# Kernel optimization log

Measured on AMD Instinct MI355X. Metric: run time of the kernel, lower is better.

The kernel has to match this reference:

```python
import jax, jax.numpy as jnp
import numpy as np

BL = 5
N = 2 ** BL  # 32; LUT is (N+1) x (N+1)


def setup_inputs() -> dict:
    key = jax.random.key(0)
    k1, k2, k3 = jax.random.split(key, 3)
    M, K, O = 512, 256, 256
    x = jax.random.uniform(k1, (M, K), dtype=jnp.float32)              # activations in [0,1)
    W = jax.random.uniform(k2, (O, K), dtype=jnp.float32) * 2.0 - 1.0  # weights in [-1,1)
    b = jax.random.uniform(k3, (O,), dtype=jnp.float32) * 2.0 - 1.0
    # Stochastic-computing multiplication LUT: A[i, j] ~ i*j/N (floored), i,j in [0, N]
    i = np.arange(N + 1, dtype=np.float32)
    lut = jnp.asarray(np.floor(np.outer(i, i) / N), dtype=jnp.float32)
    return {"x": x, "W": W, "b": b, "lut": lut}


def _sanitize(t):
    t = jnp.where(jnp.isnan(t), jnp.zeros_like(t), t)
    return jnp.where(jnp.isinf(t), jnp.ones_like(t), t)


def sc_mat_mac_p(a, b, c, lut, n):
    # Faithful port of SC_MAT_MAC_p: quantize -> LUT gather over all (row, out) pairs ->
    # sign-correct -> reduce over K -> requantize -> add quantized bias -> rescale.
    a = _sanitize(a)
    b = _sanitize(b)
    c = _sanitize(c)
    amax = jnp.abs(a).max()
    amax = jnp.where(amax == 0, jnp.ones_like(amax), amax)
    dmax = jnp.maximum(jnp.abs(b).max(), jnp.abs(c).max())
    dmax = jnp.where(dmax == 0, jnp.ones_like(dmax), dmax)
    # SBL2 = int(log2(int(N / amax))); SN2 = 2**SBL2 (truncations match torch int())
    sn2 = 2.0 ** jnp.floor(jnp.log2(jnp.floor(n / amax)))
    sn1 = 2.0 ** jnp.floor(jnp.log2(jnp.floor(n / dmax)))
    aa = (a * sn2).astype(jnp.int32)  # [M, K], |aa| <= N
    bb = (b * sn1).astype(jnp.int32)  # [O, K], |bb| <= N
    cc = (c * sn1).astype(jnp.int32)  # [O]
    # LUT gather over the full cross product (original materializes this via
    # repeat_interleave/repeat; here it is a broadcasted gather of shape [M, O, K]).
    prod = lut[jnp.abs(aa)[:, None, :], jnp.abs(bb)[None, :, :]]          # [M, O, K]
    sgn = (jnp.sign(aa)[:, None, :] * jnp.sign(bb)[None, :, :]).astype(prod.dtype)
    x9 = (sgn * prod).sum(axis=-1)                                        # [M, O]
    d = (x9 / sn2).astype(jnp.int32) + cc[None, :]
    return d.astype(jnp.float32) / sn1


def reference(x, W, b, lut):
    # out = linear(x); out.data = SC_MAT_MAC_p(...)  -> value is the SC result,
    # gradient path is the dense linear (straight-through via .data assignment).
    lin = x @ W.T + b
    p = sc_mat_mac_p(x, W, b, lut, N)
    return lin + jax.lax.stop_gradient(p - lin)
```

## Files before the change

### kernel.cpp

```cpp
#include <hip/hip_runtime.h>
#include <stdint.h>


#define MROWS 512
#define KDIM  256
#define OCOLS 256
#define NTHR  512
#define RPB   2
#define NBLK  (MROWS / RPB)
#define NWAVE (NTHR / 64)
#define E2_GUESS 5
#define E1_GUESS 5

typedef unsigned int u32x4 __attribute__((ext_vector_type(4)));

__device__ __forceinline__ void store_uc(unsigned int* p, unsigned int v) {
    asm volatile("global_store_dword %0, %1, off sc0 sc1"
                 :: "v"((unsigned long long)(uintptr_t)p), "v"(v) : "memory");
}
__device__ __forceinline__ u32x4 load_uc4(const unsigned int* p) {
    u32x4 v;
    asm volatile("global_load_dwordx4 %0, %1, off sc0 sc1\n\t"
                 "s_waitcnt vmcnt(0)"
                 : "=v"(v) : "v"((unsigned long long)(uintptr_t)p) : "memory");
    return v;
}

__device__ __forceinline__ void get_scales(float amax, float dmax, int& e2, int& e1) {
    if (amax == 0.0f) amax = 1.0f;
    if (dmax == 0.0f) dmax = 1.0f;
    float q2 = 32.0f / amax;
    float q1 = 32.0f / dmax;
    int f2 = (q2 >= 1073741824.0f) ? 0x40000000 : (int)floorf(q2);
    int f1 = (q1 >= 1073741824.0f) ? 0x40000000 : (int)floorf(q1);
    if (f2 < 1) f2 = 1;
    if (f1 < 1) f1 = 1;
    e2 = 31 - __clz(f2);
    e1 = 31 - __clz(f1);
}

__device__ __forceinline__ float max4(float4 v) {
    return fmaxf(fmaxf(fabsf(v.x), fabsf(v.y)), fmaxf(fabsf(v.z), fabsf(v.w)));
}

__device__ __forceinline__ int mac_loop(const float* __restrict__ W, int o,
                                        const unsigned int* a_sh, float sn1f,
                                        float& wmax) {
    const float4* wrow = (const float4*)(W + (size_t)o * KDIM);
    int sum = 0;
    #pragma unroll 8
    for (int kk = 0; kk < KDIM / 4; ++kk) {
        float4 wv = wrow[kk];
        unsigned int ap = a_sh[kk];
        wmax = fmaxf(wmax, max4(wv));
        float wfv[4] = {wv.x, wv.y, wv.z, wv.w};
        #pragma unroll
        for (int j = 0; j < 4; ++j) {
            int bv = (int)(wfv[j] * sn1f);
            int av = ((int)(ap << (24 - 8 * j))) >> 24;
            int s  = av * bv;
            sum += (s + ((s >> 31) & 31)) >> 5;
        }
    }
    return sum;
}

__global__ __launch_bounds__(NTHR)
void k_one(unsigned int* __restrict__ wsp, const float* __restrict__ x,
           const float* __restrict__ W, const float* __restrict__ b,
           float* __restrict__ out) {
    __shared__ unsigned int a_sh[RPB][KDIM / 4];
    __shared__ float sm[2];
    __shared__ float smd[NWAVE];
    __shared__ int s_e[2];

    const int tid  = threadIdx.x;
    const int wave = tid >> 6;
    const int bx   = blockIdx.x;
    const int m0   = bx * RPB;

    const float4* xf = (const float4*)x;
    const int o = tid & (OCOLS - 1);
    const int r = tid >> 8;
    float bo = b[o];

    float rm = 0.0f;
    if (tid < RPB * (KDIM / 4)) {
        const int rr = tid >> 6;
        const int oo = tid & 63;
        float4 xv = xf[(size_t)(m0 + rr) * (KDIM / 4) + oo];
        rm = max4(xv);
        const float g2 = (float)(1 << E2_GUESS);
        int a0 = (int)(xv.x * g2) & 0xFF;
        int a1 = (int)(xv.y * g2) & 0xFF;
        int a2 = (int)(xv.z * g2) & 0xFF;
        int a3 = (int)(xv.w * g2) & 0xFF;
        a_sh[rr][oo] = (unsigned int)(a0 | (a1 << 8) | (a2 << 16) | (a3 << 24));
    }
    if (wave < 2) {
        #pragma unroll
        for (int s = 32; s >= 1; s >>= 1)
            rm = fmaxf(rm, __shfl_xor(rm, s, 64));
        if ((tid & 63) == 0) sm[wave] = rm;
    }
    __syncthreads();
    if (tid == 0)
        store_uc(&wsp[bx], __float_as_uint(fmaxf(sm[0], sm[1])));

    float wm = 0.0f;
    int sum = mac_loop(W, o, a_sh[r], (float)(1 << E1_GUESS), wm);
    wm = fmaxf(wm, fabsf(bo));
    #pragma unroll
    for (int s = 32; s >= 1; s >>= 1)
        wm = fmaxf(wm, __shfl_xor(wm, s, 64));
    if ((tid & 63) == 0) smd[wave] = wm;
    __syncthreads();

    if (wave == 0) {
        u32x4 u;
        bool ok;
        do {
            u = load_uc4(&wsp[4 * tid]);
            ok = __all(((u.x | u.y | u.z | u.w) & 0x80000000u) == 0u);
            if (!ok) __builtin_amdgcn_s_sleep(1);
        } while (!ok);
        float va = fmaxf(fmaxf(__uint_as_float(u.x), __uint_as_float(u.y)),
                         fmaxf(__uint_as_float(u.z), __uint_as_float(u.w)));
        #pragma unroll
        for (int s = 32; s >= 1; s >>= 1)
            va = fmaxf(va, __shfl_xor(va, s, 64));
        if (tid == 0) {
            float vd = smd[0];
            #pragma unroll
            for (int i = 1; i < NWAVE; ++i) vd = fmaxf(vd, smd[i]);
            int e2, e1;
            get_scales(va, vd, e2, e1);
            s_e[0] = e2; s_e[1] = e1;
        }
    }
    __syncthreads();

    const int e2 = s_e[0];
    const int e1 = s_e[1];

    if ((e2 != E2_GUESS) | (e1 != E1_GUESS)) {
        if (tid < RPB * (KDIM / 4)) {
            const int rr = tid >> 6;
            const int oo = tid & 63;
            float4 xv = xf[(size_t)(m0 + rr) * (KDIM / 4) + oo];
            const float t2 = (float)(1 << e2);
            int a0 = (int)(xv.x * t2) & 0xFF;
            int a1 = (int)(xv.y * t2) & 0xFF;
            int a2 = (int)(xv.z * t2) & 0xFF;
            int a3 = (int)(xv.w * t2) & 0xFF;
            a_sh[rr][oo] = (unsigned int)(a0 | (a1 << 8) | (a2 << 16) | (a3 << 24));
        }
        __syncthreads();
        float dummy = 0.0f;
        sum = mac_loop(W, o, a_sh[r], (float)(1 << e1), dummy);
    }

    const float sn1f = (float)(1 << e1);
    const int cc = (int)(bo * sn1f);
    const int d  = ((sum + ((sum >> 31) & ((1 << e2) - 1))) >> e2) + cc;
    out[(size_t)(m0 + r) * OCOLS + o] = (float)d * (1.0f / sn1f);
}

extern "C" void kernel_launch(void* const* d_in, const int* in_sizes, int n_in,
                              void* d_out, int out_size, void* d_ws, size_t ws_size,
                              hipStream_t stream) {
    const float* x = (const float*)d_in[0];
    const float* W = (const float*)d_in[1];
    const float* b = (const float*)d_in[2];
    float* out = (float*)d_out;
    unsigned int* wsp = (unsigned int*)d_ws;

    k_one<<<NBLK, NTHR, 0, stream>>>(wsp, x, W, b, out);
}
```

Measured before the change: 75.36 us.

## Split K across wave lanes with coalesced W loads and shuffle reductions

The MAC loop now gives each wave 32 output columns. Each lane handles one float4 slice of K and both rows at once. W reads become coalesced across the wave, replacing the per-thread strided row reads, and each W element is reused for two rows. Per-output sums are gathered with butterfly shuffles, which adds 12 shuffles per output column. The output order is rotated by block index to spread cache traffic.

```diff
diff --git a/kernel.cpp b/kernel.cpp
--- a/kernel.cpp
+++ b/kernel.cpp
@@ -43,26 +43,42 @@
     return fmaxf(fmaxf(fabsf(v.x), fabsf(v.y)), fmaxf(fabsf(v.z), fabsf(v.w)));
 }
 
-__device__ __forceinline__ int mac_loop(const float* __restrict__ W, int o,
-                                        const unsigned int* a_sh, float sn1f,
-                                        float& wmax) {
-    const float4* wrow = (const float4*)(W + (size_t)o * KDIM);
-    int sum = 0;
-    #pragma unroll 8
-    for (int kk = 0; kk < KDIM / 4; ++kk) {
-        float4 wv = wrow[kk];
-        unsigned int ap = a_sh[kk];
+__device__ __forceinline__ int wave_mac(const float* __restrict__ W,
+                                        int obase, int lane, int rot,
+                                        unsigned int ap0, unsigned int ap1,
+                                        float sn1f, float& wmax) {
+    int av0[4], av1[4];
+    #pragma unroll
+    for (int j = 0; j < 4; ++j) {
+        av0[j] = ((int)(ap0 << (24 - 8 * j))) >> 24;
+        av1[j] = ((int)(ap1 << (24 - 8 * j))) >> 24;
+    }
+    const float4* wq = (const float4*)W;
+    int res = 0;
+    #pragma unroll 4
+    for (int i = 0; i < 32; ++i) {
+        const int io = (i + rot) & 31;
+        const int o  = obase + io;
+        float4 wv = wq[(size_t)o * (KDIM / 4) + lane];
         wmax = fmaxf(wmax, max4(wv));
-        float wfv[4] = {wv.x, wv.y, wv.z, wv.w};
+        float wf[4] = {wv.x, wv.y, wv.z, wv.w};
+        int s0 = 0, s1 = 0;
         #pragma unroll
         for (int j = 0; j < 4; ++j) {
-            int bv = (int)(wfv[j] * sn1f);
-            int av = ((int)(ap << (24 - 8 * j))) >> 24;
-            int s  = av * bv;
-            sum += (s + ((s >> 31) & 31)) >> 5;
-        }
-    }
-    return sum;
+            int bv = (int)(wf[j] * sn1f);
+            int p0 = av0[j] * bv;
+            int p1 = av1[j] * bv;
+            s0 += (p0 + ((p0 >> 31) & 31)) >> 5;
+            s1 += (p1 + ((p1 >> 31) & 31)) >> 5;
+        }
+        #pragma unroll
+        for (int sft = 32; sft >= 1; sft >>= 1) {
+            s0 += __shfl_xor(s0, sft, 64);
+            s1 += __shfl_xor(s1, sft, 64);
+        }
+        if ((lane & 31) == io) res = (lane >= 32) ? s1 : s0;
+    }
+    return res;
 }
 
 __global__ __launch_bounds__(NTHR)
@@ -75,14 +91,12 @@
     __shared__ int s_e[2];
 
     const int tid  = threadIdx.x;
-    const int wave = tid >> 6;
+    const int lane = tid & 63;
+    const int w    = tid >> 6;
     const int bx   = blockIdx.x;
     const int m0   = bx * RPB;
 
     const float4* xf = (const float4*)x;
-    const int o = tid & (OCOLS - 1);
-    const int r = tid >> 8;
-    float bo = b[o];
 
     float rm = 0.0f;
     if (tid < RPB * (KDIM / 4)) {
@@ -97,30 +111,35 @@
         int a3 = (int)(xv.w * g2) & 0xFF;
         a_sh[rr][oo] = (unsigned int)(a0 | (a1 << 8) | (a2 << 16) | (a3 << 24));
     }
-    if (wave < 2) {
+    if (w < 2) {
         #pragma unroll
         for (int s = 32; s >= 1; s >>= 1)
             rm = fmaxf(rm, __shfl_xor(rm, s, 64));
-        if ((tid & 63) == 0) sm[wave] = rm;
+        if (lane == 0) sm[w] = rm;
     }
     __syncthreads();
     if (tid == 0)
         store_uc(&wsp[bx], __float_as_uint(fmaxf(sm[0], sm[1])));
 
+    const int obase = w * 32;
+    const unsigned int ap0 = a_sh[0][lane];
+    const unsigned int ap1 = a_sh[1][lane];
     float wm = 0.0f;
-    int sum = mac_loop(W, o, a_sh[r], (float)(1 << E1_GUESS), wm);
+    int res = wave_mac(W, obase, lane, bx, ap0, ap1, (float)(1 << E1_GUESS), wm);
+
+    const float bo = b[obase + (lane & 31)];
     wm = fmaxf(wm, fabsf(bo));
     #pragma unroll
     for (int s = 32; s >= 1; s >>= 1)
         wm = fmaxf(wm, __shfl_xor(wm, s, 64));
-    if ((tid & 63) == 0) smd[wave] = wm;
+    if (lane == 0) smd[w] = wm;
     __syncthreads();
 
-    if (wave == 0) {
+    if (w == 0) {
         u32x4 u;
         bool ok;
         do {
-            u = load_uc4(&wsp[4 * tid]);
+            u = load_uc4(&wsp[4 * lane]);
             ok = __all(((u.x | u.y | u.z | u.w) & 0x80000000u) == 0u);
             if (!ok) __builtin_amdgcn_s_sleep(1);
         } while (!ok);
@@ -129,7 +148,7 @@
         #pragma unroll
         for (int s = 32; s >= 1; s >>= 1)
             va = fmaxf(va, __shfl_xor(va, s, 64));
-        if (tid == 0) {
+        if (lane == 0) {
             float vd = smd[0];
             #pragma unroll
             for (int i = 1; i < NWAVE; ++i) vd = fmaxf(vd, smd[i]);
@@ -157,13 +176,15 @@
         }
         __syncthreads();
         float dummy = 0.0f;
-        sum = mac_loop(W, o, a_sh[r], (float)(1 << e1), dummy);
+        res = wave_mac(W, obase, lane, bx, a_sh[0][lane], a_sh[1][lane],
+                       (float)(1 << e1), dummy);
     }
 
     const float sn1f = (float)(1 << e1);
     const int cc = (int)(bo * sn1f);
-    const int d  = ((sum + ((sum >> 31) & ((1 << e2) - 1))) >> e2) + cc;
-    out[(size_t)(m0 + r) * OCOLS + o] = (float)d * (1.0f / sn1f);
+    const int d  = ((res + ((res >> 31) & ((1 << e2) - 1))) >> e2) + cc;
+    out[(size_t)(m0 + (lane >> 5)) * OCOLS + obase + (lane & 31)]
+        = (float)d * (1.0f / sn1f);
 }
 
 extern "C" void kernel_launch(void* const* d_in, const int* in_sizes, int n_in,
```

After: 71.73 us. -4.8%, faster.
